# Kernel tuning notes

Hardware: AMD Instinct MI355X
Metric: run time of the kernel (lower is better)

The kernel has to match this reference:

```python
import jax, jax.numpy as jnp
import numpy as np

N, D_IN, D_OUT, K = 8192, 64, 128, 16


def setup_inputs() -> dict:
    key = jax.random.key(0)
    k1, k2, k3 = jax.random.split(key, 3)
    x = jax.random.normal(k1, (N, D_IN), dtype=jnp.float32)
    W1 = jax.random.normal(k2, (2 * D_IN, D_OUT), dtype=jnp.float32) * 0.05
    b1 = jnp.zeros((D_OUT,), dtype=jnp.float32)
    W2 = jax.random.normal(k3, (D_OUT, D_OUT), dtype=jnp.float32) * 0.05
    b2 = jnp.zeros((D_OUT,), dtype=jnp.float32)
    return {"x": x, "W1": W1, "b1": b1, "W2": W2, "b2": b2, "k": K}


def reference(x, W1, b1, W2, b2, k):
    # dynamic kNN graph (PyG knn(x, x, k) includes self as nearest neighbor)
    sq = jnp.sum(x * x, axis=-1)                      # [N]
    dist = sq[:, None] + sq[None, :] - 2.0 * (x @ x.T)  # [N, N] squared dists
    _, idx = jax.lax.top_k(-dist, k)                  # [N, k] nearest indices
    x_j = x[idx]                                      # [N, k, D_IN] gather
    x_i = jnp.broadcast_to(x[:, None, :], x_j.shape)  # [N, k, D_IN]
    e = jnp.concatenate([x_i, x_j - x_i], axis=-1)    # [N, k, 2*D_IN]
    h = jax.nn.relu(e @ W1 + b1) @ W2 + b2            # [N, k, D_OUT]
    return jnp.mean(h, axis=1)                        # mean aggregation -> [N, D_OUT]
```

## Files before the change

kernel.cpp:

```cpp
#include <hip/hip_runtime.h>

#define N 8192
#define DIN 64
#define DOUT 128
#define KNN 16
#define MSAMP 2048
#define NBX 8
#define CAND_R 64
#define CAND_C (NBX * CAND_R)
#define EPS 1.0f
#define DELTA_Q 64
#define VCAP 128
#define ROWS_PRE 16

typedef unsigned long long u64;
typedef __attribute__((ext_vector_type(8))) short bf16x8;
typedef __attribute__((ext_vector_type(4))) float floatx4;

__device__ __forceinline__ unsigned mono(float f) {
    unsigned u = __float_as_uint(f);
    return (u & 0x80000000u) ? ~u : (u | 0x80000000u);
}
__device__ __forceinline__ unsigned short f2bf(float f) {
    unsigned u = __float_as_uint(f);
    return (unsigned short)((u + 0x7FFFu + ((u >> 16) & 1u)) >> 16);
}
__device__ __forceinline__ unsigned qdist(float dist) {
    int q = (int)(dist * 128.0f) + 2;
    q = max(q, 0); return (unsigned)min(q, 65535);
}

__global__ __launch_bounds__(256) void k_pre(const float* __restrict__ x,
                                             const float* __restrict__ W1,
                                             const float* __restrict__ b1,
                                             float* __restrict__ sq,
                                             float* __restrict__ sqs,
                                             unsigned short* __restrict__ Xh,
                                             float* __restrict__ U,
                                             float* __restrict__ V) {
    __shared__ float xs[ROWS_PRE][DIN];
    int t = threadIdx.x;
    int r0 = blockIdx.x * ROWS_PRE;
    float4 xv = ((const float4*)x)[(size_t)r0 * (DIN / 4) + t];
    ((float4*)xs)[t] = xv;
    ushort4 h4;
    h4.x = f2bf(xv.x); h4.y = f2bf(xv.y);
    h4.z = f2bf(xv.z); h4.w = f2bf(xv.w);
    *(ushort4*)&Xh[r0 * DIN + t * 4] = h4;
    __syncthreads();
    if (t < ROWS_PRE) {
        const float4* xr = (const float4*)xs[t];
        float s0 = 0.f, s1 = 0.f, s2 = 0.f, s3 = 0.f;
#pragma unroll
        for (int q = 0; q < DIN / 4; ++q) {
            float4 a = xr[q];
            s0 = fmaf(a.x, a.x, s0); s1 = fmaf(a.y, a.y, s1);
            s2 = fmaf(a.z, a.z, s2); s3 = fmaf(a.w, a.w, s3);
        }
        float sv = (s0 + s1) + (s2 + s3);
        sq[r0 + t] = sv;
        if ((t & 3) == 0) sqs[(r0 + t) >> 2] = sv;
    }
    int o = t & 127, g = t >> 7;
    float aU[8], aV[8];
#pragma unroll
    for (int u = 0; u < 8; ++u) { aU[u] = 0.f; aV[u] = 0.f; }
    for (int kk = 0; kk < DIN; ++kk) {
        float whi = W1[kk * DOUT + o];
        float wlo = W1[(DIN + kk) * DOUT + o];
        float wd = whi - wlo;
#pragma unroll
        for (int u = 0; u < 8; ++u) {
            float xvv = xs[g * 8 + u][kk];
            aU[u] = fmaf(xvv, wd, aU[u]);
            aV[u] = fmaf(xvv, wlo, aV[u]);
        }
    }
    float bb = b1[o];
#pragma unroll
    for (int u = 0; u < 8; ++u) {
        int r = r0 + g * 8 + u;
        U[(size_t)r * DOUT + o] = aU[u] + bb;
        V[(size_t)r * DOUT + o] = aV[u];
    }
}

__global__ __launch_bounds__(256, 4) void k_presample(const unsigned short* __restrict__ Xh,
                                                      const float* __restrict__ sq,
                                                      const float* __restrict__ sqs,
                                                      unsigned short* __restrict__ prekq) {
    __shared__ __align__(16) short ldsH[64 * 72];
    int tid = threadIdx.x, w = tid >> 6, l = tid & 63;
    int m = l & 15, ko = (l >> 4) * 8, quad = l >> 4;
    int bx = blockIdx.x;
    int rt = blockIdx.y * 4 + w;
    int irow = rt * 16 + m;
    size_t arow = (size_t)irow * DIN;
    bf16x8 iH0 = *(const bf16x8*)(Xh + arow + ko);
    bf16x8 iH1 = *(const bf16x8*)(Xh + arow + 32 + ko);
    float si = sq[irow];
    int srw = tid >> 3, scol8 = (tid & 7) * 8;
    for (int st = 0; st < 4; ++st) {
        int sbase = bx * 256 + st * 64;
        __syncthreads();
        *(bf16x8*)&ldsH[srw * 72 + scol8] =
            *(const bf16x8*)(Xh + (size_t)(4 * (sbase + srw)) * DIN + scol8);
        *(bf16x8*)&ldsH[(srw + 32) * 72 + scol8] =
            *(const bf16x8*)(Xh + (size_t)(4 * (sbase + srw + 32)) * DIN + scol8);
        __syncthreads();
#pragma unroll
        for (int it = 0; it < 4; ++it) {
            int br = it * 16 + m;
            bf16x8 sH0 = *(const bf16x8*)&ldsH[br * 72 + ko];
            bf16x8 sH1 = *(const bf16x8*)&ldsH[br * 72 + 32 + ko];
            floatx4 acc = {0.f, 0.f, 0.f, 0.f};
            acc = __builtin_amdgcn_mfma_f32_16x16x32_bf16(sH0, iH0, acc, 0, 0, 0);
            acc = __builtin_amdgcn_mfma_f32_16x16x32_bf16(sH1, iH1, acc, 0, 0, 0);
            int sc0 = sbase + it * 16 + quad * 4;
            float4 sj = *(const float4*)(sqs + sc0);
            u64 pk;
            {
                unsigned q0 = qdist(fmaf(-2.0f, acc[0], si + sj.x));
                unsigned q1 = qdist(fmaf(-2.0f, acc[1], si + sj.y));
                unsigned q2 = qdist(fmaf(-2.0f, acc[2], si + sj.z));
                unsigned q3 = qdist(fmaf(-2.0f, acc[3], si + sj.w));
                pk = (u64)q0 | ((u64)q1 << 16) | ((u64)q2 << 32) | ((u64)q3 << 48);
            }
            *(u64*)(prekq + (size_t)irow * MSAMP + sc0) = pk;
        }
    }
}

__global__ __launch_bounds__(256, 4) void k_tau(const unsigned short* __restrict__ prekq,
                                                float* __restrict__ tauf) {
    int w = threadIdx.x >> 6, l = threadIdx.x & 63;
    int row = blockIdx.x * 4 + w;
    unsigned v[MSAMP / 64];
#pragma unroll
    for (int u = 0; u < MSAMP / 64; ++u)
        v[u] = prekq[(size_t)row * MSAMP + l + 64 * u];
    unsigned p = 0;
#pragma unroll
    for (int b = 15; b >= 0; --b) {
        unsigned c16 = p | (1u << b);
        int cnt = 0;
#pragma unroll
        for (int u = 0; u < MSAMP / 64; ++u)
            cnt += __popcll(__ballot(v[u] < c16));
        if (cnt < 16) p = c16;
    }
    if (l == 0) tauf[row] = (float)p * (1.0f / 128.0f);
}

__global__ __launch_bounds__(256, 4) void k_main(const unsigned short* __restrict__ Xh,
                                                 const float* __restrict__ sq,
                                                 const float* __restrict__ tauf,
                                                 unsigned* __restrict__ cand,
                                                 unsigned* __restrict__ cntpart) {
    __shared__ __align__(16) short ldsH[64 * 72];
    int tid = threadIdx.x, w = tid >> 6, l = tid & 63;
    int m = l & 15, ko = (l >> 4) * 8;
    int bx = blockIdx.x;
    int rt = blockIdx.y * 4 + w;
    size_t arow = (size_t)(rt * 16 + m) * DIN;
    bf16x8 aH0 = *(const bf16x8*)(Xh + arow + ko);
    bf16x8 aH1 = *(const bf16x8*)(Xh + arow + 32 + ko);
    int rg[4]; float T[4]; float si[4]; int rowcnt[4];
#pragma unroll
    for (int reg = 0; reg < 4; ++reg) {
        rg[reg] = rt * 16 + (l >> 4) * 4 + reg;
        si[reg] = sq[rg[reg]];
        T[reg] = tauf[rg[reg]] + EPS - si[reg];
        rowcnt[reg] = 0;
    }
    int qs = l & 48;
    unsigned lmask = (1u << (l & 15)) - 1u;
    int srw = tid >> 3, scol8 = (tid & 7) * 8;

    for (int st = 0; st < 16; ++st) {
        int jbase = bx * 1024 + st * 64;
        __syncthreads();
        *(bf16x8*)&ldsH[srw * 72 + scol8] =
            *(const bf16x8*)(Xh + (size_t)(jbase + srw) * DIN + scol8);
        *(bf16x8*)&ldsH[(srw + 32) * 72 + scol8] =
            *(const bf16x8*)(Xh + (size_t)(jbase + srw + 32) * DIN + scol8);
        __syncthreads();
#pragma unroll
        for (int it = 0; it < 4; ++it) {
            int br = it * 16 + m;
            bf16x8 bH0 = *(const bf16x8*)&ldsH[br * 72 + ko];
            bf16x8 bH1 = *(const bf16x8*)&ldsH[br * 72 + 32 + ko];
            floatx4 acc = {0.f, 0.f, 0.f, 0.f};
            acc = __builtin_amdgcn_mfma_f32_16x16x32_bf16(aH0, bH0, acc, 0, 0, 0);
            acc = __builtin_amdgcn_mfma_f32_16x16x32_bf16(aH1, bH1, acc, 0, 0, 0);
            int jcol = jbase + it * 16 + m;
            float sqj = sq[jcol];
#pragma unroll
            for (int reg = 0; reg < 4; ++reg) {
                float tv = fmaf(-2.0f, acc[reg], sqj);
                bool pass = tv <= T[reg];
                u64 bal = __ballot(pass);
                if (bal) {
                    unsigned m16 = (unsigned)((bal >> qs) & 0xFFFFull);
                    if (pass) {
                        int slot = rowcnt[reg] + __popc(m16 & lmask);
                        if (slot < CAND_R)
                            cand[(size_t)rg[reg] * CAND_C + bx * CAND_R + slot] =
                                (qdist(tv + si[reg]) << 16) | (unsigned)jcol;
                    }
                    rowcnt[reg] += __popc(m16);
                }
            }
        }
    }
    if ((l & 15) == 0) {
#pragma unroll
        for (int reg = 0; reg < 4; ++reg)
            cntpart[rg[reg] * NBX + bx] = (unsigned)min(rowcnt[reg], CAND_R);
    }
}

__global__ __launch_bounds__(256) void k_exact(const float* __restrict__ x,
                                               const float* __restrict__ sq,
                                               const unsigned* __restrict__ cntpart,
                                               const unsigned* __restrict__ cand,
                                               int* __restrict__ knn) {
    __shared__ unsigned cj[4][CAND_C];
    __shared__ unsigned short vlist[4][VCAP];
    __shared__ u64 ekeys[4][VCAP];
    int w = threadIdx.x >> 6, l = threadIdx.x & 63;
    int row = blockIdx.x * 4 + w;
    int base = 0;
#pragma unroll
    for (int b = 0; b < NBX; ++b) {
        int c = (int)cntpart[row * NBX + b];
        c = min(c, CAND_R);
        if (l < c) cj[w][base + l] = cand[(size_t)row * CAND_C + b * CAND_R + l];
        base += c;
    }
    __syncthreads();
    unsigned kk[CAND_C / 64], qq[CAND_C / 64];
#pragma unroll
    for (int u = 0; u < CAND_C / 64; ++u) {
        int idx = l + 64 * u;
        kk[u] = (idx < base) ? cj[w][idx] : 0xFFFFFFFFu;
        qq[u] = (idx < base) ? (kk[u] >> 16) : 0xFFFFFFFFu;
    }
    unsigned p = 0;
#pragma unroll
    for (int b = 15; b >= 0; --b) {
        unsigned c16 = p | (1u << b);
        int cnt = 0;
#pragma unroll
        for (int u = 0; u < CAND_C / 64; ++u)
            cnt += __popcll(__ballot(qq[u] < c16));
        if (cnt < 16) p = c16;
    }
    unsigned thr = p + DELTA_Q;
    int nv = 0;
    u64 lm = (l == 63) ? 0xFFFFFFFFFFFFFFFFull >> 1 : (1ull << l) - 1ull;
#pragma unroll
    for (int u = 0; u < CAND_C / 64; ++u) {
        bool pred = qq[u] <= thr;
        u64 bal = __ballot(pred);
        int slot = nv + __popcll(bal & lm);
        if (pred && slot < VCAP) vlist[w][slot] = (unsigned short)(kk[u] & 0xFFFFu);
        nv += __popcll(bal);
    }
    nv = min(nv, VCAP);
    __syncthreads();
    float sqi = sq[row];
    const float* xi = x + (size_t)row * DIN;
#pragma unroll
    for (int r = 0; r < VCAP / 64; ++r) {
        int v = l + 64 * r;
        if (v < nv) {
            int j = (int)vlist[w][v];
            const float4* bj = (const float4*)(x + (size_t)j * DIN);
            float4 rb[16];
#pragma unroll
            for (int q = 0; q < DIN / 4; ++q) rb[q] = bj[q];
            float s0 = 0.f, s1 = 0.f, s2 = 0.f, s3 = 0.f;
#pragma unroll
            for (int q = 0; q < DIN / 4; ++q) {
                s0 = fmaf(xi[4 * q + 0], rb[q].x, s0);
                s1 = fmaf(xi[4 * q + 1], rb[q].y, s1);
                s2 = fmaf(xi[4 * q + 2], rb[q].z, s2);
                s3 = fmaf(xi[4 * q + 3], rb[q].w, s3);
            }
            float d = (s0 + s1) + (s2 + s3);
            float dist = fmaf(-2.0f, d, sqi + sq[j]);
            ekeys[w][v] = ((u64)mono(dist) << 32) | (unsigned)j;
        }
    }
#pragma unroll
    for (int r = 0; r < VCAP / 64; ++r) {
        int v = l + 64 * r;
        if (v < nv) {
            u64 mykey = ekeys[w][v];
            int rank = 0;
            for (int i = 0; i < nv; ++i)
                rank += (ekeys[w][i] < mykey) ? 1 : 0;
            if (rank < KNN)
                knn[row * KNN + rank] = (int)(unsigned)(mykey & 0xFFFFFFFFull);
        }
    }
}

__global__ __launch_bounds__(256) void k_aggout(const float* __restrict__ U,
                                                const float* __restrict__ V,
                                                const int* __restrict__ knn,
                                                const float* __restrict__ W2,
                                                const float* __restrict__ b2,
                                                float* __restrict__ out) {
    __shared__ float ag[8][DOUT];
    __shared__ float w2t[32 * DOUT];
    int t = threadIdx.x;
    int o = t & 127, g = t >> 7;
    int i0 = blockIdx.x * 8 + g * 4;
#pragma unroll
    for (int r = 0; r < 4; ++r) {
        int i = i0 + r;
        float u = U[(size_t)i * DOUT + o];
        const int* nb = knn + i * KNN;
        float acc = 0.f;
#pragma unroll
        for (int q = 0; q < KNN; ++q)
            acc += fmaxf(u + V[(size_t)nb[q] * DOUT + o], 0.0f);
        ag[g * 4 + r][o] = acc * (1.0f / KNN);
    }
    float a2[4] = {0.f, 0.f, 0.f, 0.f};
#pragma unroll
    for (int tile = 0; tile < 4; ++tile) {
        __syncthreads();
#pragma unroll
        for (int u = 0; u < 4; ++u)
            ((float4*)w2t)[t + u * 256] =
                ((const float4*)(W2 + tile * 32 * DOUT))[t + u * 256];
        __syncthreads();
#pragma unroll 8
        for (int kk = 0; kk < 32; ++kk) {
            float wv = w2t[kk * DOUT + o];
#pragma unroll
            for (int r = 0; r < 4; ++r)
                a2[r] = fmaf(ag[g * 4 + r][tile * 32 + kk], wv, a2[r]);
        }
    }
    float bb = b2[o];
#pragma unroll
    for (int r = 0; r < 4; ++r)
        out[(size_t)(i0 + r) * DOUT + o] = a2[r] + bb;
}

extern "C" void kernel_launch(void* const* d_in, const int* in_sizes, int n_in,
                              void* d_out, int out_size, void* d_ws, size_t ws_size,
                              hipStream_t stream) {
    const float* x  = (const float*)d_in[0];
    const float* W1 = (const float*)d_in[1];
    const float* b1 = (const float*)d_in[2];
    const float* W2 = (const float*)d_in[3];
    const float* b2 = (const float*)d_in[4];
    float* out = (float*)d_out;

    char* ws = (char*)d_ws;
    float*          sq      = (float*)(ws);
    float*          sqs     = (float*)(ws + 32768);
    float*          tauf    = (float*)(ws + 40960);
    int*            knn     = (int*)(ws + 73728);
    unsigned short* Xh      = (unsigned short*)(ws + 655360);
    unsigned*       cntpart = (unsigned*)(ws + 1703936);
    float*          U       = (float*)(ws + 2097152);
    float*          V       = (float*)(ws + 6291456);
    char*           region  = ws + 10485760;
    unsigned short* prekq   = (unsigned short*)region;
    unsigned*       cand    = (unsigned*)region;

    k_pre<<<N / ROWS_PRE, 256, 0, stream>>>(x, W1, b1, sq, sqs, Xh, U, V);
    k_presample<<<dim3(8, 128), 256, 0, stream>>>(Xh, sq, sqs, prekq);
    k_tau<<<N / 4, 256, 0, stream>>>(prekq, tauf);
    k_main<<<dim3(NBX, 128), 256, 0, stream>>>(Xh, sq, tauf, cand, cntpart);
    k_exact<<<N / 4, 256, 0, stream>>>(x, sq, cntpart, cand, knn);
    k_aggout<<<N / 8, 256, 0, stream>>>(U, V, knn, W2, b2, out);
}
```

Baseline: 184.0 us.

## Fuse exact kNN selection with aggregation and use LDS atomics for candidate slots

Merges the exact top-k kernel with the neighbor aggregation and W2 projection into a single kernel, so kNN indices stay in shared memory and one launch plus a global round trip is removed. The candidate compaction in the main distance kernel replaces per-row ballot/popcount bookkeeping with shared-memory atomic counters. Per-block candidate capacity grows from 64 to 96, raising shared-memory use and candidate-load work in the exact stage. The fused kernel reads W2 straight from global memory without LDS tiling and computes 2 rows per thread instead of 4, which lowers W2 reuse. Some intra-wave __syncthreads calls are dropped, so correctness now relies on each wave touching only its own shared-memory slices.

Result: no change. 186.5 us (+1.3%).

```diff
diff --git a/kernel.cpp b/kernel.cpp
--- a/kernel.cpp
+++ b/kernel.cpp
@@ -6,7 +6,7 @@
 #define KNN 16
 #define MSAMP 2048
 #define NBX 8
-#define CAND_R 64
+#define CAND_R 96
 #define CAND_C (NBX * CAND_R)
 #define EPS 1.0f
 #define DELTA_Q 64
@@ -118,14 +118,11 @@
             acc = __builtin_amdgcn_mfma_f32_16x16x32_bf16(sH1, iH1, acc, 0, 0, 0);
             int sc0 = sbase + it * 16 + quad * 4;
             float4 sj = *(const float4*)(sqs + sc0);
-            u64 pk;
-            {
-                unsigned q0 = qdist(fmaf(-2.0f, acc[0], si + sj.x));
-                unsigned q1 = qdist(fmaf(-2.0f, acc[1], si + sj.y));
-                unsigned q2 = qdist(fmaf(-2.0f, acc[2], si + sj.z));
-                unsigned q3 = qdist(fmaf(-2.0f, acc[3], si + sj.w));
-                pk = (u64)q0 | ((u64)q1 << 16) | ((u64)q2 << 32) | ((u64)q3 << 48);
-            }
+            unsigned q0 = qdist(fmaf(-2.0f, acc[0], si + sj.x));
+            unsigned q1 = qdist(fmaf(-2.0f, acc[1], si + sj.y));
+            unsigned q2 = qdist(fmaf(-2.0f, acc[2], si + sj.z));
+            unsigned q3 = qdist(fmaf(-2.0f, acc[3], si + sj.w));
+            u64 pk = (u64)q0 | ((u64)q1 << 16) | ((u64)q2 << 32) | ((u64)q3 << 48);
             *(u64*)(prekq + (size_t)irow * MSAMP + sc0) = pk;
         }
     }
@@ -158,23 +155,23 @@
                                                  unsigned* __restrict__ cand,
                                                  unsigned* __restrict__ cntpart) {
     __shared__ __align__(16) short ldsH[64 * 72];
+    __shared__ int cnt[64];
     int tid = threadIdx.x, w = tid >> 6, l = tid & 63;
-    int m = l & 15, ko = (l >> 4) * 8;
+    int m = l & 15, ko = (l >> 4) * 8, quad = l >> 4;
     int bx = blockIdx.x;
     int rt = blockIdx.y * 4 + w;
+    if (tid < 64) cnt[tid] = 0;
     size_t arow = (size_t)(rt * 16 + m) * DIN;
     bf16x8 aH0 = *(const bf16x8*)(Xh + arow + ko);
     bf16x8 aH1 = *(const bf16x8*)(Xh + arow + 32 + ko);
-    int rg[4]; float T[4]; float si[4]; int rowcnt[4];
+    int rg[4], lrow[4]; float T[4]; float si[4];
 #pragma unroll
     for (int reg = 0; reg < 4; ++reg) {
-        rg[reg] = rt * 16 + (l >> 4) * 4 + reg;
+        rg[reg] = rt * 16 + quad * 4 + reg;
+        lrow[reg] = w * 16 + quad * 4 + reg;
         si[reg] = sq[rg[reg]];
         T[reg] = tauf[rg[reg]] + EPS - si[reg];
-        rowcnt[reg] = 0;
-    }
-    int qs = l & 48;
-    unsigned lmask = (1u << (l & 15)) - 1u;
+    }
     int srw = tid >> 3, scol8 = (tid & 7) * 8;
 
     for (int st = 0; st < 16; ++st) {
@@ -198,47 +195,47 @@
 #pragma unroll
             for (int reg = 0; reg < 4; ++reg) {
                 float tv = fmaf(-2.0f, acc[reg], sqj);
-                bool pass = tv <= T[reg];
-                u64 bal = __ballot(pass);
-                if (bal) {
-                    unsigned m16 = (unsigned)((bal >> qs) & 0xFFFFull);
-                    if (pass) {
-                        int slot = rowcnt[reg] + __popc(m16 & lmask);
-                        if (slot < CAND_R)
-                            cand[(size_t)rg[reg] * CAND_C + bx * CAND_R + slot] =
-                                (qdist(tv + si[reg]) << 16) | (unsigned)jcol;
-                    }
-                    rowcnt[reg] += __popc(m16);
+                if (tv <= T[reg]) {
+                    int slot = atomicAdd(&cnt[lrow[reg]], 1);
+                    if (slot < CAND_R)
+                        cand[(size_t)rg[reg] * CAND_C + bx * CAND_R + slot] =
+                            (qdist(tv + si[reg]) << 16) | (unsigned)jcol;
                 }
             }
         }
     }
-    if ((l & 15) == 0) {
-#pragma unroll
-        for (int reg = 0; reg < 4; ++reg)
-            cntpart[rg[reg] * NBX + bx] = (unsigned)min(rowcnt[reg], CAND_R);
-    }
-}
-
-__global__ __launch_bounds__(256) void k_exact(const float* __restrict__ x,
-                                               const float* __restrict__ sq,
-                                               const unsigned* __restrict__ cntpart,
-                                               const unsigned* __restrict__ cand,
-                                               int* __restrict__ knn) {
+    __syncthreads();
+    if (tid < 64)
+        cntpart[(blockIdx.y * 64 + tid) * NBX + bx] =
+            (unsigned)min(cnt[tid], CAND_R);
+}
+
+__global__ __launch_bounds__(256) void k_exact_agg(const float* __restrict__ x,
+                                                   const float* __restrict__ sq,
+                                                   const unsigned* __restrict__ cntpart,
+                                                   const unsigned* __restrict__ cand,
+                                                   const float* __restrict__ U,
+                                                   const float* __restrict__ V,
+                                                   const float* __restrict__ W2,
+                                                   const float* __restrict__ b2,
+                                                   float* __restrict__ out) {
     __shared__ unsigned cj[4][CAND_C];
     __shared__ unsigned short vlist[4][VCAP];
     __shared__ u64 ekeys[4][VCAP];
-    int w = threadIdx.x >> 6, l = threadIdx.x & 63;
+    __shared__ int knnl[4][KNN];
+    __shared__ float ag[4][DOUT];
+    int t = threadIdx.x;
+    int w = t >> 6, l = t & 63;
     int row = blockIdx.x * 4 + w;
     int base = 0;
 #pragma unroll
     for (int b = 0; b < NBX; ++b) {
         int c = (int)cntpart[row * NBX + b];
         c = min(c, CAND_R);
-        if (l < c) cj[w][base + l] = cand[(size_t)row * CAND_C + b * CAND_R + l];
+        for (int s = l; s < c; s += 64)
+            cj[w][base + s] = cand[(size_t)row * CAND_C + b * CAND_R + s];
         base += c;
     }
-    __syncthreads();
     unsigned kk[CAND_C / 64], qq[CAND_C / 64];
 #pragma unroll
     for (int u = 0; u < CAND_C / 64; ++u) {
@@ -268,7 +265,6 @@
         nv += __popcll(bal);
     }
     nv = min(nv, VCAP);
-    __syncthreads();
     float sqi = sq[row];
     const float* xi = x + (size_t)row * DIN;
 #pragma unroll
@@ -302,54 +298,33 @@
             for (int i = 0; i < nv; ++i)
                 rank += (ekeys[w][i] < mykey) ? 1 : 0;
             if (rank < KNN)
-                knn[row * KNN + rank] = (int)(unsigned)(mykey & 0xFFFFFFFFull);
-        }
-    }
-}
-
-__global__ __launch_bounds__(256) void k_aggout(const float* __restrict__ U,
-                                                const float* __restrict__ V,
-                                                const int* __restrict__ knn,
-                                                const float* __restrict__ W2,
-                                                const float* __restrict__ b2,
-                                                float* __restrict__ out) {
-    __shared__ float ag[8][DOUT];
-    __shared__ float w2t[32 * DOUT];
-    int t = threadIdx.x;
+                knnl[w][rank] = (int)(unsigned)(mykey & 0xFFFFFFFFull);
+        }
+    }
+    __syncthreads();
     int o = t & 127, g = t >> 7;
-    int i0 = blockIdx.x * 8 + g * 4;
-#pragma unroll
-    for (int r = 0; r < 4; ++r) {
-        int i = i0 + r;
-        float u = U[(size_t)i * DOUT + o];
-        const int* nb = knn + i * KNN;
+    int i0 = blockIdx.x * 4;
+#pragma unroll
+    for (int rr = 0; rr < 2; ++rr) {
+        int rl = g * 2 + rr;
+        float u = U[(size_t)(i0 + rl) * DOUT + o];
         float acc = 0.f;
 #pragma unroll
         for (int q = 0; q < KNN; ++q)
-            acc += fmaxf(u + V[(size_t)nb[q] * DOUT + o], 0.0f);
-        ag[g * 4 + r][o] = acc * (1.0f / KNN);
-    }
-    float a2[4] = {0.f, 0.f, 0.f, 0.f};
-#pragma unroll
-    for (int tile = 0; tile < 4; ++tile) {
-        __syncthreads();
-#pragma unroll
-        for (int u = 0; u < 4; ++u)
-            ((float4*)w2t)[t + u * 256] =
-                ((const float4*)(W2 + tile * 32 * DOUT))[t + u * 256];
-        __syncthreads();
-#pragma unroll 8
-        for (int kk = 0; kk < 32; ++kk) {
-            float wv = w2t[kk * DOUT + o];
-#pragma unroll
-            for (int r = 0; r < 4; ++r)
-                a2[r] = fmaf(ag[g * 4 + r][tile * 32 + kk], wv, a2[r]);
-        }
+            acc += fmaxf(u + V[(size_t)knnl[rl][q] * DOUT + o], 0.0f);
+        ag[rl][o] = acc * (1.0f / KNN);
+    }
+    __syncthreads();
+    float a2[2] = {0.f, 0.f};
+#pragma unroll 4
+    for (int k = 0; k < DOUT; ++k) {
+        float wv = W2[k * DOUT + o];
+        a2[0] = fmaf(ag[g * 2 + 0][k], wv, a2[0]);
+        a2[1] = fmaf(ag[g * 2 + 1][k], wv, a2[1]);
     }
     float bb = b2[o];
-#pragma unroll
-    for (int r = 0; r < 4; ++r)
-        out[(size_t)(i0 + r) * DOUT + o] = a2[r] + bb;
+    out[(size_t)(i0 + g * 2 + 0) * DOUT + o] = a2[0] + bb;
+    out[(size_t)(i0 + g * 2 + 1) * DOUT + o] = a2[1] + bb;
 }
 
 extern "C" void kernel_launch(void* const* d_in, const int* in_sizes, int n_in,
@@ -366,7 +341,6 @@
     float*          sq      = (float*)(ws);
     float*          sqs     = (float*)(ws + 32768);
     float*          tauf    = (float*)(ws + 40960);
-    int*            knn     = (int*)(ws + 73728);
     unsigned short* Xh      = (unsigned short*)(ws + 655360);
     unsigned*       cntpart = (unsigned*)(ws + 1703936);
     float*          U       = (float*)(ws + 2097152);
@@ -379,6 +353,5 @@
     k_presample<<<dim3(8, 128), 256, 0, stream>>>(Xh, sq, sqs, prekq);
     k_tau<<<N / 4, 256, 0, stream>>>(prekq, tauf);
     k_main<<<dim3(NBX, 128), 256, 0, stream>>>(Xh, sq, tauf, cand, cntpart);
-    k_exact<<<N / 4, 256, 0, stream>>>(x, sq, cntpart, cand, knn);
-    k_aggout<<<N / 8, 256, 0, stream>>>(U, V, knn, W2, b2, out);
-}
+    k_exact_agg<<<N / 4, 256, 0, stream>>>(x, sq, cntpart, cand, U, V, W2, b2, out);
+}
```

## Fuse presample distance quantization and tau selection into one kernel via LDS

Applied to the files above, without the earlier changes.

Merges the sampled-distance kernel and the per-row threshold selection kernel into a single kernel. Each block handles 16 rows, computes their quantized distances to all 2048 samples into shared memory, and then runs the bitwise radix threshold search directly from LDS. This removes the 32 MB global round trip of the prekq buffer and one kernel launch. In exchange each block uses about 73 KB of LDS, which limits occupancy, and the 512-block grid is smaller than before.

Result: slower. 199.5 us (+8.4%).

```diff
diff --git a/kernel.cpp b/kernel.cpp
--- a/kernel.cpp
+++ b/kernel.cpp
@@ -11,6 +11,7 @@
 #define EPS 1.0f
 #define DELTA_Q 64
 #define VCAP 128
+#define PSTR 2052
 #define ROWS_PRE 16
 
 typedef unsigned long long u64;
@@ -85,71 +86,64 @@
     }
 }
 
-__global__ __launch_bounds__(256, 4) void k_presample(const unsigned short* __restrict__ Xh,
-                                                      const float* __restrict__ sq,
-                                                      const float* __restrict__ sqs,
-                                                      unsigned short* __restrict__ prekq) {
+__global__ __launch_bounds__(256) void k_pretau(const unsigned short* __restrict__ Xh,
+                                                const float* __restrict__ sq,
+                                                const float* __restrict__ sqs,
+                                                float* __restrict__ tauf) {
     __shared__ __align__(16) short ldsH[64 * 72];
+    __shared__ unsigned short prek[16][PSTR];
     int tid = threadIdx.x, w = tid >> 6, l = tid & 63;
     int m = l & 15, ko = (l >> 4) * 8, quad = l >> 4;
-    int bx = blockIdx.x;
-    int rt = blockIdx.y * 4 + w;
-    int irow = rt * 16 + m;
-    size_t arow = (size_t)irow * DIN;
-    bf16x8 iH0 = *(const bf16x8*)(Xh + arow + ko);
-    bf16x8 iH1 = *(const bf16x8*)(Xh + arow + 32 + ko);
-    float si = sq[irow];
+    int rt = blockIdx.x;
+    size_t arow = (size_t)(rt * 16 + m) * DIN;
+    bf16x8 aH0 = *(const bf16x8*)(Xh + arow + ko);
+    bf16x8 aH1 = *(const bf16x8*)(Xh + arow + 32 + ko);
+    float si[4];
+#pragma unroll
+    for (int reg = 0; reg < 4; ++reg) si[reg] = sq[rt * 16 + quad * 4 + reg];
     int srw = tid >> 3, scol8 = (tid & 7) * 8;
-    for (int st = 0; st < 4; ++st) {
-        int sbase = bx * 256 + st * 64;
+    for (int st = 0; st < 32; ++st) {
+        int sbase = st * 64;
         __syncthreads();
         *(bf16x8*)&ldsH[srw * 72 + scol8] =
             *(const bf16x8*)(Xh + (size_t)(4 * (sbase + srw)) * DIN + scol8);
         *(bf16x8*)&ldsH[(srw + 32) * 72 + scol8] =
             *(const bf16x8*)(Xh + (size_t)(4 * (sbase + srw + 32)) * DIN + scol8);
         __syncthreads();
-#pragma unroll
-        for (int it = 0; it < 4; ++it) {
-            int br = it * 16 + m;
-            bf16x8 sH0 = *(const bf16x8*)&ldsH[br * 72 + ko];
-            bf16x8 sH1 = *(const bf16x8*)&ldsH[br * 72 + 32 + ko];
-            floatx4 acc = {0.f, 0.f, 0.f, 0.f};
-            acc = __builtin_amdgcn_mfma_f32_16x16x32_bf16(sH0, iH0, acc, 0, 0, 0);
-            acc = __builtin_amdgcn_mfma_f32_16x16x32_bf16(sH1, iH1, acc, 0, 0, 0);
-            int sc0 = sbase + it * 16 + quad * 4;
-            float4 sj = *(const float4*)(sqs + sc0);
-            u64 pk;
-            {
-                unsigned q0 = qdist(fmaf(-2.0f, acc[0], si + sj.x));
-                unsigned q1 = qdist(fmaf(-2.0f, acc[1], si + sj.y));
-                unsigned q2 = qdist(fmaf(-2.0f, acc[2], si + sj.z));
-                unsigned q3 = qdist(fmaf(-2.0f, acc[3], si + sj.w));
-                pk = (u64)q0 | ((u64)q1 << 16) | ((u64)q2 << 32) | ((u64)q3 << 48);
-            }
-            *(u64*)(prekq + (size_t)irow * MSAMP + sc0) = pk;
-        }
-    }
-}
-
-__global__ __launch_bounds__(256, 4) void k_tau(const unsigned short* __restrict__ prekq,
-                                                float* __restrict__ tauf) {
-    int w = threadIdx.x >> 6, l = threadIdx.x & 63;
-    int row = blockIdx.x * 4 + w;
-    unsigned v[MSAMP / 64];
-#pragma unroll
-    for (int u = 0; u < MSAMP / 64; ++u)
-        v[u] = prekq[(size_t)row * MSAMP + l + 64 * u];
-    unsigned p = 0;
-#pragma unroll
-    for (int b = 15; b >= 0; --b) {
-        unsigned c16 = p | (1u << b);
-        int cnt = 0;
+        int br = w * 16 + m;
+        bf16x8 bH0 = *(const bf16x8*)&ldsH[br * 72 + ko];
+        bf16x8 bH1 = *(const bf16x8*)&ldsH[br * 72 + 32 + ko];
+        floatx4 acc = {0.f, 0.f, 0.f, 0.f};
+        acc = __builtin_amdgcn_mfma_f32_16x16x32_bf16(aH0, bH0, acc, 0, 0, 0);
+        acc = __builtin_amdgcn_mfma_f32_16x16x32_bf16(aH1, bH1, acc, 0, 0, 0);
+        int scol = sbase + w * 16 + m;
+        float sqj = sqs[scol];
+#pragma unroll
+        for (int reg = 0; reg < 4; ++reg) {
+            float dist = fmaf(-2.0f, acc[reg], si[reg] + sqj);
+            prek[quad * 4 + reg][scol] = (unsigned short)qdist(dist);
+        }
+    }
+    __syncthreads();
+#pragma unroll
+    for (int rr = 0; rr < 4; ++rr) {
+        int lr = w * 4 + rr;
+        unsigned v[MSAMP / 64];
 #pragma unroll
         for (int u = 0; u < MSAMP / 64; ++u)
-            cnt += __popcll(__ballot(v[u] < c16));
-        if (cnt < 16) p = c16;
-    }
-    if (l == 0) tauf[row] = (float)p * (1.0f / 128.0f);
+            v[u] = prek[lr][l + 64 * u];
+        unsigned p = 0;
+#pragma unroll
+        for (int b = 15; b >= 0; --b) {
+            unsigned c16 = p | (1u << b);
+            int cnt = 0;
+#pragma unroll
+            for (int u = 0; u < MSAMP / 64; ++u)
+                cnt += __popcll(__ballot(v[u] < c16));
+            if (cnt < 16) p = c16;
+        }
+        if (l == 0) tauf[rt * 16 + lr] = (float)p * (1.0f / 128.0f);
+    }
 }
 
 __global__ __launch_bounds__(256, 4) void k_main(const unsigned short* __restrict__ Xh,
@@ -371,13 +365,10 @@
     unsigned*       cntpart = (unsigned*)(ws + 1703936);
     float*          U       = (float*)(ws + 2097152);
     float*          V       = (float*)(ws + 6291456);
-    char*           region  = ws + 10485760;
-    unsigned short* prekq   = (unsigned short*)region;
-    unsigned*       cand    = (unsigned*)region;
+    unsigned*       cand    = (unsigned*)(ws + 10485760);
 
     k_pre<<<N / ROWS_PRE, 256, 0, stream>>>(x, W1, b1, sq, sqs, Xh, U, V);
-    k_presample<<<dim3(8, 128), 256, 0, stream>>>(Xh, sq, sqs, prekq);
-    k_tau<<<N / 4, 256, 0, stream>>>(prekq, tauf);
+    k_pretau<<<N / 16, 256, 0, stream>>>(Xh, sq, sqs, tauf);
     k_main<<<dim3(NBX, 128), 256, 0, stream>>>(Xh, sq, tauf, cand, cntpart);
     k_exact<<<N / 4, 256, 0, stream>>>(x, sq, cntpart, cand, knn);
     k_aggout<<<N / 8, 256, 0, stream>>>(U, V, knn, W2, b2, out);
```
